# Optimization experiments

Hardware: AMD Instinct MI355X
Metric: run time of the kernel (lower is better)

Reference implementation:

```python
import jax, jax.numpy as jnp
import numpy as np

V, D, T_MAX, H, L = 32000, 1024, 1024, 16, 8
HD = D // H
DFF = 4 * D
EPS = 1e-5


def _pos_encoding(T, d_model, dtype=jnp.float32):
    pos = jnp.arange(T, dtype=jnp.float32)[:, None]                      # [T,1]
    div = jnp.exp(jnp.arange(0, d_model, 2, dtype=jnp.float32) * (-jnp.log(10000.0) / d_model))
    pe = jnp.zeros((T, d_model), dtype=jnp.float32)
    pe = pe.at[:, 0::2].set(jnp.sin(pos * div))
    pe = pe.at[:, 1::2].set(jnp.cos(pos * div))
    return pe.astype(dtype)


def _layernorm(x, g, b):
    mu = jnp.mean(x, axis=-1, keepdims=True)
    var = jnp.mean(jnp.square(x - mu), axis=-1, keepdims=True)
    return (x - mu) * jax.lax.rsqrt(var + EPS) * g + b


def setup_inputs() -> dict:
    key = jax.random.key(0)
    ks = jax.random.split(key, 9)
    s = 0.02
    return {
        "idx": jax.random.randint(ks[0], (2, 1024), 0, V),
        "embed": jax.random.normal(ks[1], (V, D), jnp.float32) * s,
        "Wqkv": jax.random.normal(ks[2], (L, D, 3 * D), jnp.float32) * s,
        "Wproj": jax.random.normal(ks[3], (L, D, D), jnp.float32) * s,
        "bproj": jnp.zeros((L, D), jnp.float32),
        "ln1_g": jnp.ones((L, D), jnp.float32),
        "ln1_b": jnp.zeros((L, D), jnp.float32),
        "ln2_g": jnp.ones((L, D), jnp.float32),
        "ln2_b": jnp.zeros((L, D), jnp.float32),
        "W1": jax.random.normal(ks[4], (L, D, DFF), jnp.float32) * s,
        "b1": jnp.zeros((L, DFF), jnp.float32),
        "W2": jax.random.normal(ks[5], (L, DFF, D), jnp.float32) * s,
        "b2": jnp.zeros((L, D), jnp.float32),
        "lnf_g": jnp.ones((D,), jnp.float32),
        "lnf_b": jnp.zeros((D,), jnp.float32),
        "Whead": jax.random.normal(ks[6], (D, V), jnp.float32) * s,
    }


def _attn(x, Wqkv, Wproj, bproj):
    B, T, C = x.shape
    qkv = (x @ Wqkv).reshape(B, T, 3, H, HD)
    q, k, v = [jnp.transpose(qkv[:, :, i], (0, 2, 1, 3)) for i in range(3)]  # [B,H,T,HD]
    scores = jnp.einsum('bhqd,bhkd->bhqk', q, k) * (HD ** -0.5)
    mask = jnp.tril(jnp.ones((T, T), dtype=bool))
    scores = jnp.where(mask, scores, -jnp.inf)
    w = jax.nn.softmax(scores, axis=-1)
    out = jnp.einsum('bhqk,bhkd->bhqd', w, v)
    out = jnp.transpose(out, (0, 2, 1, 3)).reshape(B, T, C)
    return out @ Wproj + bproj


def reference(idx, embed, Wqkv, Wproj, bproj, ln1_g, ln1_b, ln2_g, ln2_b,
              W1, b1, W2, b2, lnf_g, lnf_b, Whead):
    idx = idx[:, :T_MAX]
    T = idx.shape[1]
    x = embed[idx] + _pos_encoding(T, D)[None]          # [B,T,D]
    for l in range(L):
        x = x + _attn(_layernorm(x, ln1_g[l], ln1_b[l]), Wqkv[l], Wproj[l], bproj[l])
        h = _layernorm(x, ln2_g[l], ln2_b[l])
        x = x + jax.nn.relu(h @ W1[l] + b1[l]) @ W2[l] + b2[l]
    x = _layernorm(x, lnf_g, lnf_b)
    return x @ Whead                                     # [B,T,V]
```

## Files before the change

kernel.cpp:

```cpp
#include <hip/hip_runtime.h>
#include <cstddef>

#define DM    1024
#define TSEQ  1024
#define NB    2
#define NHEAD 16
#define HDIM  64
#define NLAYER 8
#define DFFN  4096
#define NVOC  32000
#define NROWS (NB*TSEQ)

typedef __attribute__((ext_vector_type(8))) short short8;
typedef __attribute__((ext_vector_type(4))) float f32x4;

static __device__ __forceinline__ unsigned short f2bf(float f) {
    union { float f; unsigned int u; } v; v.f = f;
    unsigned int r = v.u + 0x7FFF + ((v.u >> 16) & 1);
    return (unsigned short)(r >> 16);
}

static __device__ __forceinline__ void gload_lds16(const void* g, void* l) {
    __builtin_amdgcn_global_load_lds(
        (const __attribute__((address_space(1))) unsigned int*)g,
        (__attribute__((address_space(3))) unsigned int*)l, 16, 0, 0);
}

__global__ __launch_bounds__(256)
void embed_pos_k(const int* __restrict__ idx, const float* __restrict__ embed,
                 float* __restrict__ x)
{
    int row = blockIdx.x;
    int t   = row & (TSEQ - 1);
    int tid = threadIdx.x;
    int token = idx[row];
    const float* er = embed + (size_t)token * DM;
    float* xr = x + (size_t)row * DM;
    const float neg_ln1e4_over_d = -9.210340371976184f / (float)DM;
    for (int i = tid; i < DM; i += 256) {
        int half = i >> 1;
        float div = expf((float)(2 * half) * neg_ln1e4_over_d);
        float ang = (float)t * div;
        float pe = (i & 1) ? cosf(ang) : sinf(ang);
        xr[i] = er[i] + pe;
    }
}

__global__ __launch_bounds__(256)
void layernorm_k(const float* __restrict__ x, const float* __restrict__ g,
                 const float* __restrict__ b, unsigned short* __restrict__ y)
{
    int row = blockIdx.x;
    int tid = threadIdx.x;
    const float* xr = x + (size_t)row * DM;
    unsigned short* yr = y + (size_t)row * DM;
    float vals[4];
    float s = 0.f;
    #pragma unroll
    for (int i = 0; i < 4; ++i) { vals[i] = xr[tid + 256 * i]; s += vals[i]; }
    __shared__ float red[256];
    red[tid] = s; __syncthreads();
    for (int st = 128; st > 0; st >>= 1) {
        if (tid < st) red[tid] += red[tid + st];
        __syncthreads();
    }
    float mu = red[0] * (1.f / DM);
    __syncthreads();
    float v = 0.f;
    #pragma unroll
    for (int i = 0; i < 4; ++i) { float d = vals[i] - mu; v += d * d; }
    red[tid] = v; __syncthreads();
    for (int st = 128; st > 0; st >>= 1) {
        if (tid < st) red[tid] += red[tid + st];
        __syncthreads();
    }
    float rstd = rsqrtf(red[0] * (1.f / DM) + 1e-5f);
    #pragma unroll
    for (int i = 0; i < 4; ++i) {
        int c = tid + 256 * i;
        yr[c] = f2bf((vals[i] - mu) * rstd * g[c] + b[c]);
    }
}

__global__ __launch_bounds__(256)
void reduce_ln_k(const float* __restrict__ P, int nsplit, const float* __restrict__ bias,
                 float* __restrict__ X, const float* __restrict__ g,
                 const float* __restrict__ b, unsigned short* __restrict__ XN)
{
    const int row = blockIdx.x;
    const int tid = threadIdx.x;
    const size_t off4 = (size_t)row * 256 + tid;
    const size_t tot4 = (size_t)NROWS * 256;

    float4 v = *((const float4*)X + off4);
    float4 bb = *((const float4*)bias + tid);
    v.x += bb.x; v.y += bb.y; v.z += bb.z; v.w += bb.w;
    for (int s = 0; s < nsplit; ++s) {
        float4 p = *((const float4*)P + s * tot4 + off4);
        v.x += p.x; v.y += p.y; v.z += p.z; v.w += p.w;
    }
    *((float4*)X + off4) = v;

    __shared__ float red[256];
    red[tid] = v.x + v.y + v.z + v.w;
    __syncthreads();
    for (int st = 128; st > 0; st >>= 1) {
        if (tid < st) red[tid] += red[tid + st];
        __syncthreads();
    }
    float mu = red[0] * (1.f / DM);
    __syncthreads();
    float4 d = make_float4(v.x - mu, v.y - mu, v.z - mu, v.w - mu);
    red[tid] = d.x * d.x + d.y * d.y + d.z * d.z + d.w * d.w;
    __syncthreads();
    for (int st = 128; st > 0; st >>= 1) {
        if (tid < st) red[tid] += red[tid + st];
        __syncthreads();
    }
    float rstd = rsqrtf(red[0] * (1.f / DM) + 1e-5f);
    float4 gg = *((const float4*)g + tid);
    float4 bbn = *((const float4*)b + tid);
    unsigned short o[4];
    o[0] = f2bf(d.x * rstd * gg.x + bbn.x);
    o[1] = f2bf(d.y * rstd * gg.y + bbn.y);
    o[2] = f2bf(d.z * rstd * gg.z + bbn.z);
    o[3] = f2bf(d.w * rstd * gg.w + bbn.w);
    *(ushort4*)(XN + (size_t)row * DM + tid * 4) = *(ushort4*)o;
}

__global__ __launch_bounds__(256)
void convt_k(const float* __restrict__ src, unsigned short* __restrict__ dst,
             int K, int N)
{
    __shared__ __align__(16) unsigned short T[64][72];
    const int tid = threadIdx.x;
    const int n0 = blockIdx.x * 64, k0 = blockIdx.y * 64;
    const float* s = src + (size_t)blockIdx.z * K * N;
    unsigned short* d = dst + (size_t)blockIdx.z * K * N;
    #pragma unroll
    for (int q = 0; q < 4; ++q) {
        int f4 = tid + q * 256;
        int kk = f4 >> 4, nn = (f4 & 15) * 4;
        float4 v = *(const float4*)(s + (size_t)(k0 + kk) * N + n0 + nn);
        int swz = ((nn >> 2) & 7) << 3;
        T[nn + 0][kk ^ swz] = f2bf(v.x);
        T[nn + 1][kk ^ swz] = f2bf(v.y);
        T[nn + 2][kk ^ swz] = f2bf(v.z);
        T[nn + 3][kk ^ swz] = f2bf(v.w);
    }
    __syncthreads();
    #pragma unroll
    for (int q = 0; q < 2; ++q) {
        int s8 = tid + q * 256;
        int nn = s8 >> 3, kc = (s8 & 7) * 8;
        int swz = ((nn >> 2) & 7) << 3;
        *(short8*)(d + (size_t)(n0 + nn) * K + k0 + kc) =
            *(const short8*)&T[nn][kc ^ swz];
    }
}

template<int BM, int BN, bool OUT_BF16>
__global__ __launch_bounds__(256, 4)
void gemm_tn(const unsigned short* __restrict__ A, const unsigned short* __restrict__ BT,
             const float* __restrict__ bias, const float* __restrict__ residual,
             void* __restrict__ Cout, int M, int N, int K, int KS, int relu)
{
    constexpr int FRM = BM / 32;
    constexpr int FRN = BN / 32;
    constexpr int NIA = BM / 64;
    constexpr int NIB = BN / 64;
    constexpr int NLD = NIA + NIB;
    __shared__ __align__(16) unsigned short As[3][BM][32];
    __shared__ __align__(16) unsigned short Bs[3][BN][32];

    const int tid = threadIdx.x;
    const int lane = tid & 63;
    const int w = tid >> 6;
    const int wr = w >> 1, wc = w & 1;
    const int l16 = lane & 15, g = lane >> 4;

    const int nby = M / BM;
    const int nwg = (N / BN) * nby;
    const int cpx = nwg >> 3;
    const int bid = blockIdx.x;
    const int sbid = (bid & 7) * cpx + (bid >> 3);
    const int row0 = (sbid % nby) * BM;
    const int col0 = (sbid / nby) * BN;

    const int srowA = w * (BM / 4) + (lane >> 2);
    const int srowB = w * (BN / 4) + (lane >> 2);
    const int scol = (((lane & 3) ^ ((lane >> 3) & 3)) << 3);
    const int rslot = ((g ^ ((l16 >> 1) & 3)) << 3);
    const int ldst = (lane & 3) << 3;

    const unsigned short* ga = A  + (size_t)(row0 + srowA) * KS + (size_t)blockIdx.y * K + scol;
    const unsigned short* gb = BT + (size_t)(col0 + srowB) * KS + (size_t)blockIdx.y * K + scol;

    f32x4 acc[FRM][FRN] = {};
    const int NT = K >> 5;

    #pragma unroll
    for (int i = 0; i < NIA; ++i)
        gload_lds16(ga + (size_t)(i * 16) * KS, &As[0][srowA + i * 16][ldst]);
    #pragma unroll
    for (int i = 0; i < NIB; ++i)
        gload_lds16(gb + (size_t)(i * 16) * KS, &Bs[0][srowB + i * 16][ldst]);

    for (int t = 0; t < NT; ++t) {
        const int rb = t % 3;
        if (t + 1 < NT) {
            const int wb = (t + 1) % 3;
            const int ko = (t + 1) * 32;
            #pragma unroll
            for (int i = 0; i < NIA; ++i)
                gload_lds16(ga + ko + (size_t)(i * 16) * KS, &As[wb][srowA + i * 16][ldst]);
            #pragma unroll
            for (int i = 0; i < NIB; ++i)
                gload_lds16(gb + ko + (size_t)(i * 16) * KS, &Bs[wb][srowB + i * 16][ldst]);
            asm volatile("s_waitcnt vmcnt(%0)" :: "i"(NLD) : "memory");
        } else {
            asm volatile("s_waitcnt vmcnt(0)" ::: "memory");
        }
        __builtin_amdgcn_s_barrier();

        short8 af[FRM], bf[FRN];
        #pragma unroll
        for (int i = 0; i < FRM; ++i)
            af[i] = *(const short8*)&As[rb][wr * (BM / 2) + i * 16 + l16][rslot];
        #pragma unroll
        for (int j = 0; j < FRN; ++j)
            bf[j] = *(const short8*)&Bs[rb][wc * (BN / 2) + j * 16 + l16][rslot];
        __builtin_amdgcn_s_setprio(1);
        #pragma unroll
        for (int i = 0; i < FRM; ++i)
            #pragma unroll
            for (int j = 0; j < FRN; ++j)
                acc[i][j] = __builtin_amdgcn_mfma_f32_16x16x32_bf16(af[i], bf[j], acc[i][j], 0, 0, 0);
        __builtin_amdgcn_s_setprio(0);
    }

    float* Cf = (float*)Cout + (size_t)blockIdx.y * M * N;
    #pragma unroll
    for (int i = 0; i < FRM; ++i) {
        #pragma unroll
        for (int j = 0; j < FRN; ++j) {
            #pragma unroll
            for (int r = 0; r < 4; ++r) {
                int row = row0 + wr * (BM / 2) + i * 16 + g * 4 + r;
                int col = col0 + wc * (BN / 2) + j * 16 + l16;
                float v = acc[i][j][r];
                if (bias)     v += bias[col];
                if (residual) v += residual[(size_t)row * N + col];
                if (relu)     v = fmaxf(v, 0.f);
                if (OUT_BF16) ((unsigned short*)Cout)[(size_t)row * N + col] = f2bf(v);
                else          Cf[(size_t)row * N + col] = v;
            }
        }
    }
}

__global__ __launch_bounds__(256)
void attn_flash_k(const unsigned short* __restrict__ qkv, unsigned short* __restrict__ out)
{
    __shared__ unsigned short Ks[128][72];
    __shared__ unsigned short Vt[64][136];
    __shared__ unsigned short Ps[4][16][136];

    const int tid = threadIdx.x;
    const int lane = tid & 63;
    const int w = tid >> 6;
    const int l16 = lane & 15, g = lane >> 4;
    const int h = blockIdx.y;
    const int b = blockIdx.z;

    const size_t rstr = 3 * DM;
    const unsigned short* base = qkv + (size_t)b * TSEQ * rstr + h * HDIM;

    const int krow = tid >> 1, kcol = (tid & 1) * 32;
    const int vkv = tid & 127, vdh = (tid >> 7) * 32;

    short8 kreg[4], vreg[4];

    #pragma unroll
    for (int pass = 0; pass < 2; ++pass) {
        const int qb = pass ? (15 - (int)blockIdx.x) : (int)blockIdx.x;
        const int q0 = qb * 64;
        const int nt = (qb >> 1) + 1;

        const int qrow_w = q0 + w * 16 + l16;
        short8 aq0 = *(const short8*)(base + (size_t)qrow_w * rstr + g * 8);
        short8 aq1 = *(const short8*)(base + (size_t)qrow_w * rstr + 32 + g * 8);

        f32x4 acc_o[4] = {};
        float m_r[4] = {-INFINITY, -INFINITY, -INFINITY, -INFINITY};
        float l_r[4] = {};

        {
            const unsigned short* kb = base + (size_t)krow * rstr + DM + kcol;
            #pragma unroll
            for (int i = 0; i < 4; ++i) kreg[i] = *(const short8*)(kb + i * 8);
            const unsigned short* vb = base + (size_t)vkv * rstr + 2 * DM + vdh;
            #pragma unroll
            for (int i = 0; i < 4; ++i) vreg[i] = *(const short8*)(vb + i * 8);
        }

        for (int t = 0; t < nt; ++t) {
            #pragma unroll
            for (int i = 0; i < 4; ++i) *(short8*)&Ks[krow][kcol + i * 8] = kreg[i];
            #pragma unroll
            for (int jj = 0; jj < 4; ++jj)
                #pragma unroll
                for (int j = 0; j < 8; ++j)
                    Vt[vdh + jj * 8 + j][vkv] = (unsigned short)vreg[jj][j];
            __syncthreads();

            if (t + 1 < nt) {
                const int kv0n = (t + 1) * 128;
                const unsigned short* kb = base + (size_t)(kv0n + krow) * rstr + DM + kcol;
                #pragma unroll
                for (int i = 0; i < 4; ++i) kreg[i] = *(const short8*)(kb + i * 8);
                const unsigned short* vb = base + (size_t)(kv0n + vkv) * rstr + 2 * DM + vdh;
                #pragma unroll
                for (int i = 0; i < 4; ++i) vreg[i] = *(const short8*)(vb + i * 8);
            }

            const int kv0 = t * 128;
            f32x4 acc_s[8] = {};
            #pragma unroll
            for (int ks = 0; ks < 8; ++ks) {
                short8 bk0 = *(const short8*)&Ks[ks * 16 + l16][g * 8];
                short8 bk1 = *(const short8*)&Ks[ks * 16 + l16][32 + g * 8];
                acc_s[ks] = __builtin_amdgcn_mfma_f32_16x16x32_bf16(aq0, bk0, acc_s[ks], 0, 0, 0);
                acc_s[ks] = __builtin_amdgcn_mfma_f32_16x16x32_bf16(aq1, bk1, acc_s[ks], 0, 0, 0);
            }
            const bool need_mask = (kv0 + 127 > q0 + w * 16);
            float alpha[4];
            #pragma unroll
            for (int r = 0; r < 4; ++r) {
                const int q_abs = q0 + w * 16 + g * 4 + r;
                float s[8];
                #pragma unroll
                for (int ks = 0; ks < 8; ++ks) {
                    s[ks] = acc_s[ks][r] * 0.125f;
                    if (need_mask && (kv0 + ks * 16 + l16 > q_abs)) s[ks] = -INFINITY;
                }
                float pm = fmaxf(fmaxf(fmaxf(s[0], s[1]), fmaxf(s[2], s[3])),
                                 fmaxf(fmaxf(s[4], s[5]), fmaxf(s[6], s[7])));
                #pragma unroll
                for (int msk = 1; msk <= 8; msk <<= 1)
                    pm = fmaxf(pm, __shfl_xor(pm, msk));
                float mnew = fmaxf(m_r[r], pm);
                alpha[r] = __expf(m_r[r] - mnew);
                m_r[r] = mnew;
                float p[8], psum = 0.f;
                #pragma unroll
                for (int ks = 0; ks < 8; ++ks) {
                    p[ks] = (s[ks] == -INFINITY) ? 0.f : __expf(s[ks] - mnew);
                    psum += p[ks];
                }
                #pragma unroll
                for (int msk = 1; msk <= 8; msk <<= 1)
                    psum += __shfl_xor(psum, msk);
                l_r[r] = l_r[r] * alpha[r] + psum;
                #pragma unroll
                for (int ks = 0; ks < 8; ++ks)
                    Ps[w][g * 4 + r][ks * 16 + l16] = f2bf(p[ks]);
            }
            #pragma unroll
            for (int ds = 0; ds < 4; ++ds)
                #pragma unroll
                for (int r = 0; r < 4; ++r)
                    acc_o[ds][r] *= alpha[r];
            short8 ap[4];
            #pragma unroll
            for (int kk = 0; kk < 4; ++kk)
                ap[kk] = *(const short8*)&Ps[w][l16][kk * 32 + g * 8];
            #pragma unroll
            for (int ds = 0; ds < 4; ++ds) {
                #pragma unroll
                for (int kk = 0; kk < 4; ++kk) {
                    short8 bv = *(const short8*)&Vt[ds * 16 + l16][kk * 32 + g * 8];
                    acc_o[ds] = __builtin_amdgcn_mfma_f32_16x16x32_bf16(ap[kk], bv, acc_o[ds], 0, 0, 0);
                }
            }
            __syncthreads();
        }

        #pragma unroll
        for (int ds = 0; ds < 4; ++ds)
            #pragma unroll
            for (int r = 0; r < 4; ++r) {
                int row = q0 + w * 16 + g * 4 + r;
                out[((size_t)b * TSEQ + row) * DM + h * HDIM + ds * 16 + l16] =
                    f2bf(acc_o[ds][r] * (1.f / l_r[r]));
            }
    }
}

extern "C" void kernel_launch(void* const* d_in, const int* in_sizes, int n_in,
                              void* d_out, int out_size, void* d_ws, size_t ws_size,
                              hipStream_t stream)
{
    const int*   idx    = (const int*)  d_in[0];
    const float* embed  = (const float*)d_in[1];
    const float* Wqkv   = (const float*)d_in[2];
    const float* Wproj  = (const float*)d_in[3];
    const float* bproj  = (const float*)d_in[4];
    const float* ln1_g  = (const float*)d_in[5];
    const float* ln1_b  = (const float*)d_in[6];
    const float* ln2_g  = (const float*)d_in[7];
    const float* ln2_b  = (const float*)d_in[8];
    const float* W1     = (const float*)d_in[9];
    const float* b1     = (const float*)d_in[10];
    const float* W2     = (const float*)d_in[11];
    const float* b2     = (const float*)d_in[12];
    const float* lnf_g  = (const float*)d_in[13];
    const float* lnf_b  = (const float*)d_in[14];
    const float* Whead  = (const float*)d_in[15];
    float* out = (float*)d_out;

    float* X = (float*)d_ws;
    float* PK = X + (size_t)NROWS * DM;
    unsigned short* u = (unsigned short*)(PK + (size_t)4 * NROWS * DM);
    unsigned short* XN     = u;  u += (size_t)NROWS * DM;
    unsigned short* QKVb   = u;  u += (size_t)NROWS * 3 * DM;
    unsigned short* ATT    = u;  u += (size_t)NROWS * DM;
    unsigned short* FFH    = u;  u += (size_t)NROWS * DFFN;
    unsigned short* WqkvT  = u;  u += (size_t)NLAYER * 3 * DM * DM;
    unsigned short* WprojT = u;  u += (size_t)NLAYER * DM * DM;
    unsigned short* W1T    = u;  u += (size_t)NLAYER * DFFN * DM;
    unsigned short* W2T    = u;  u += (size_t)NLAYER * DM * DFFN;
    unsigned short* WheadT = u;  u += (size_t)NVOC * DM;

    convt_k<<<dim3(3 * DM / 64, DM / 64, NLAYER), 256, 0, stream>>>(Wqkv,  WqkvT,  DM,   3 * DM);
    convt_k<<<dim3(DM / 64,     DM / 64, NLAYER), 256, 0, stream>>>(Wproj, WprojT, DM,   DM);
    convt_k<<<dim3(DFFN / 64,   DM / 64, NLAYER), 256, 0, stream>>>(W1,    W1T,    DM,   DFFN);
    convt_k<<<dim3(DM / 64,   DFFN / 64, NLAYER), 256, 0, stream>>>(W2,    W2T,    DFFN, DM);
    convt_k<<<dim3(NVOC / 64,   DM / 64, 1),      256, 0, stream>>>(Whead, WheadT, DM,   NVOC);

    embed_pos_k<<<NROWS, 256, 0, stream>>>(idx, embed, X);
    layernorm_k<<<NROWS, 256, 0, stream>>>(X, ln1_g, ln1_b, XN);

    for (int l = 0; l < NLAYER; ++l) {
        const unsigned short* wqkvT_l  = WqkvT  + (size_t)l * 3 * DM * DM;
        const unsigned short* wprojT_l = WprojT + (size_t)l * DM * DM;
        const unsigned short* w1T_l    = W1T    + (size_t)l * DFFN * DM;
        const unsigned short* w2T_l    = W2T    + (size_t)l * DM * DFFN;
        const float* bproj_l = bproj + (size_t)l * DM;
        const float* b1_l = b1 + (size_t)l * DFFN;
        const float* b2_l = b2 + (size_t)l * DM;

        {
            int nwg = (NROWS / 128) * (3 * DM / 64);
            gemm_tn<128, 64, true><<<nwg, 256, 0, stream>>>(XN, wqkvT_l, nullptr, nullptr,
                                                            QKVb, NROWS, 3 * DM, DM, DM, 0);
        }
        {
            dim3 grid(TSEQ / 128, NHEAD, NB);
            attn_flash_k<<<grid, 256, 0, stream>>>(QKVb, ATT);
        }
        {
            dim3 grid((NROWS / 128) * (DM / 64), 2);
            gemm_tn<128, 64, false><<<grid, 256, 0, stream>>>(ATT, wprojT_l, nullptr, nullptr,
                                                              PK, NROWS, DM, 512, DM, 0);
            reduce_ln_k<<<NROWS, 256, 0, stream>>>(PK, 2, bproj_l, X,
                                                   ln2_g + (size_t)l * DM,
                                                   ln2_b + (size_t)l * DM, XN);
        }
        {
            int nwg = (NROWS / 128) * (DFFN / 64);
            gemm_tn<128, 64, true><<<nwg, 256, 0, stream>>>(XN, w1T_l, b1_l, nullptr,
                                                            FFH, NROWS, DFFN, DM, DM, 1);
        }
        {
            dim3 grid((NROWS / 128) * (DM / 64), 4);
            gemm_tn<128, 64, false><<<grid, 256, 0, stream>>>(FFH, w2T_l, nullptr, nullptr,
                                                              PK, NROWS, DM, 1024, DFFN, 0);
            const float* ng = (l + 1 < NLAYER) ? ln1_g + (size_t)(l + 1) * DM : lnf_g;
            const float* nb = (l + 1 < NLAYER) ? ln1_b + (size_t)(l + 1) * DM : lnf_b;
            reduce_ln_k<<<NROWS, 256, 0, stream>>>(PK, 4, b2_l, X, ng, nb, XN);
        }
    }

    {
        int nwg = (NROWS / 128) * (NVOC / 64);
        gemm_tn<128, 64, false><<<nwg, 256, 0, stream>>>(XN, WheadT, nullptr, nullptr,
                                                         out, NROWS, NVOC, DM, DM, 0);
    }
}
```

Baseline: 1.729 ms.

## Split attention into one q-block per workgroup and use 128x128 tiles for LM head

The attention kernel no longer runs two passes (q-block b and its mirror) per workgroup. It now launches 512 workgroups with a flat id that maps heavy q-blocks first, which gives more parallelism and a longest-first schedule. The online softmax now skips rescaling unless the max grows by more than 8, and it drops the explicit -inf check. The LM-head GEMM switches to a 128x128 tile variant without the occupancy hint, which raises data reuse per tile but may lower occupancy. The GEMM body is turned into a shared macro.

```diff
diff --git a/kernel.cpp b/kernel.cpp
--- a/kernel.cpp
+++ b/kernel.cpp
@@ -159,104 +159,107 @@
     }
 }
 
-template<int BM, int BN, bool OUT_BF16>
+#define GEMM_BODY(BM, BN)                                                        \
+    constexpr int FRM = (BM) / 32;                                               \
+    constexpr int FRN = (BN) / 32;                                               \
+    constexpr int NIA = (BM) / 64;                                               \
+    constexpr int NIB = (BN) / 64;                                               \
+    constexpr int NLD = NIA + NIB;                                               \
+    __shared__ __align__(16) unsigned short As[3][BM][32];                       \
+    __shared__ __align__(16) unsigned short Bs[3][BN][32];                       \
+    const int tid = threadIdx.x;                                                 \
+    const int lane = tid & 63;                                                   \
+    const int w = tid >> 6;                                                      \
+    const int wr = w >> 1, wc = w & 1;                                           \
+    const int l16 = lane & 15, g = lane >> 4;                                    \
+    const int nby = M / (BM);                                                    \
+    const int nwg = (N / (BN)) * nby;                                            \
+    const int cpx = nwg >> 3;                                                    \
+    const int bid = blockIdx.x;                                                  \
+    const int sbid = (bid & 7) * cpx + (bid >> 3);                               \
+    const int row0 = (sbid % nby) * (BM);                                        \
+    const int col0 = (sbid / nby) * (BN);                                        \
+    const int srowA = w * ((BM) / 4) + (lane >> 2);                              \
+    const int srowB = w * ((BN) / 4) + (lane >> 2);                              \
+    const int scol = (((lane & 3) ^ ((lane >> 3) & 3)) << 3);                    \
+    const int rslot = ((g ^ ((l16 >> 1) & 3)) << 3);                             \
+    const int ldst = (lane & 3) << 3;                                            \
+    const unsigned short* ga = A  + (size_t)(row0 + srowA) * KS + (size_t)blockIdx.y * K + scol; \
+    const unsigned short* gb = BT + (size_t)(col0 + srowB) * KS + (size_t)blockIdx.y * K + scol; \
+    f32x4 acc[FRM][FRN] = {};                                                    \
+    const int NT = K >> 5;                                                       \
+    _Pragma("unroll")                                                            \
+    for (int i = 0; i < NIA; ++i)                                                \
+        gload_lds16(ga + (size_t)(i * 16) * KS, &As[0][srowA + i * 16][ldst]);   \
+    _Pragma("unroll")                                                            \
+    for (int i = 0; i < NIB; ++i)                                                \
+        gload_lds16(gb + (size_t)(i * 16) * KS, &Bs[0][srowB + i * 16][ldst]);   \
+    for (int t = 0; t < NT; ++t) {                                               \
+        const int rb = t % 3;                                                    \
+        if (t + 1 < NT) {                                                        \
+            const int wb = (t + 1) % 3;                                          \
+            const int ko = (t + 1) * 32;                                         \
+            _Pragma("unroll")                                                    \
+            for (int i = 0; i < NIA; ++i)                                        \
+                gload_lds16(ga + ko + (size_t)(i * 16) * KS, &As[wb][srowA + i * 16][ldst]); \
+            _Pragma("unroll")                                                    \
+            for (int i = 0; i < NIB; ++i)                                        \
+                gload_lds16(gb + ko + (size_t)(i * 16) * KS, &Bs[wb][srowB + i * 16][ldst]); \
+            asm volatile("s_waitcnt vmcnt(%0)" :: "i"(NLD) : "memory");          \
+        } else {                                                                 \
+            asm volatile("s_waitcnt vmcnt(0)" ::: "memory");                     \
+        }                                                                        \
+        __builtin_amdgcn_s_barrier();                                            \
+        short8 af[FRM], bf[FRN];                                                 \
+        _Pragma("unroll")                                                        \
+        for (int i = 0; i < FRM; ++i)                                            \
+            af[i] = *(const short8*)&As[rb][wr * ((BM) / 2) + i * 16 + l16][rslot]; \
+        _Pragma("unroll")                                                        \
+        for (int j = 0; j < FRN; ++j)                                            \
+            bf[j] = *(const short8*)&Bs[rb][wc * ((BN) / 2) + j * 16 + l16][rslot]; \
+        __builtin_amdgcn_s_setprio(1);                                           \
+        _Pragma("unroll")                                                        \
+        for (int i = 0; i < FRM; ++i)                                            \
+            _Pragma("unroll")                                                    \
+            for (int j = 0; j < FRN; ++j)                                        \
+                acc[i][j] = __builtin_amdgcn_mfma_f32_16x16x32_bf16(af[i], bf[j], acc[i][j], 0, 0, 0); \
+        __builtin_amdgcn_s_setprio(0);                                           \
+    }                                                                            \
+    float* Cf = (float*)Cout + (size_t)blockIdx.y * M * N;                       \
+    _Pragma("unroll")                                                            \
+    for (int i = 0; i < FRM; ++i) {                                              \
+        _Pragma("unroll")                                                        \
+        for (int j = 0; j < FRN; ++j) {                                          \
+            _Pragma("unroll")                                                    \
+            for (int r = 0; r < 4; ++r) {                                        \
+                int row = row0 + wr * ((BM) / 2) + i * 16 + g * 4 + r;           \
+                int col = col0 + wc * ((BN) / 2) + j * 16 + l16;                 \
+                float v = acc[i][j][r];                                          \
+                if (bias)     v += bias[col];                                    \
+                if (residual) v += residual[(size_t)row * N + col];              \
+                if (relu)     v = fmaxf(v, 0.f);                                 \
+                if (OUT_BF16) ((unsigned short*)Cout)[(size_t)row * N + col] = f2bf(v); \
+                else          Cf[(size_t)row * N + col] = v;                     \
+            }                                                                    \
+        }                                                                        \
+    }
+
+template<bool OUT_BF16>
+__global__ __launch_bounds__(256)
+void gemm_big(const unsigned short* __restrict__ A, const unsigned short* __restrict__ BT,
+              const float* __restrict__ bias, const float* __restrict__ residual,
+              void* __restrict__ Cout, int M, int N, int K, int KS, int relu)
+{
+    GEMM_BODY(128, 128)
+}
+
+template<bool OUT_BF16>
 __global__ __launch_bounds__(256, 4)
-void gemm_tn(const unsigned short* __restrict__ A, const unsigned short* __restrict__ BT,
+void gemm_sm(const unsigned short* __restrict__ A, const unsigned short* __restrict__ BT,
              const float* __restrict__ bias, const float* __restrict__ residual,
              void* __restrict__ Cout, int M, int N, int K, int KS, int relu)
 {
-    constexpr int FRM = BM / 32;
-    constexpr int FRN = BN / 32;
-    constexpr int NIA = BM / 64;
-    constexpr int NIB = BN / 64;
-    constexpr int NLD = NIA + NIB;
-    __shared__ __align__(16) unsigned short As[3][BM][32];
-    __shared__ __align__(16) unsigned short Bs[3][BN][32];
-
-    const int tid = threadIdx.x;
-    const int lane = tid & 63;
-    const int w = tid >> 6;
-    const int wr = w >> 1, wc = w & 1;
-    const int l16 = lane & 15, g = lane >> 4;
-
-    const int nby = M / BM;
-    const int nwg = (N / BN) * nby;
-    const int cpx = nwg >> 3;
-    const int bid = blockIdx.x;
-    const int sbid = (bid & 7) * cpx + (bid >> 3);
-    const int row0 = (sbid % nby) * BM;
-    const int col0 = (sbid / nby) * BN;
-
-    const int srowA = w * (BM / 4) + (lane >> 2);
-    const int srowB = w * (BN / 4) + (lane >> 2);
-    const int scol = (((lane & 3) ^ ((lane >> 3) & 3)) << 3);
-    const int rslot = ((g ^ ((l16 >> 1) & 3)) << 3);
-    const int ldst = (lane & 3) << 3;
-
-    const unsigned short* ga = A  + (size_t)(row0 + srowA) * KS + (size_t)blockIdx.y * K + scol;
-    const unsigned short* gb = BT + (size_t)(col0 + srowB) * KS + (size_t)blockIdx.y * K + scol;
-
-    f32x4 acc[FRM][FRN] = {};
-    const int NT = K >> 5;
-
-    #pragma unroll
-    for (int i = 0; i < NIA; ++i)
-        gload_lds16(ga + (size_t)(i * 16) * KS, &As[0][srowA + i * 16][ldst]);
-    #pragma unroll
-    for (int i = 0; i < NIB; ++i)
-        gload_lds16(gb + (size_t)(i * 16) * KS, &Bs[0][srowB + i * 16][ldst]);
-
-    for (int t = 0; t < NT; ++t) {
-        const int rb = t % 3;
-        if (t + 1 < NT) {
-            const int wb = (t + 1) % 3;
-            const int ko = (t + 1) * 32;
-            #pragma unroll
-            for (int i = 0; i < NIA; ++i)
-                gload_lds16(ga + ko + (size_t)(i * 16) * KS, &As[wb][srowA + i * 16][ldst]);
-            #pragma unroll
-            for (int i = 0; i < NIB; ++i)
-                gload_lds16(gb + ko + (size_t)(i * 16) * KS, &Bs[wb][srowB + i * 16][ldst]);
-            asm volatile("s_waitcnt vmcnt(%0)" :: "i"(NLD) : "memory");
-        } else {
-            asm volatile("s_waitcnt vmcnt(0)" ::: "memory");
-        }
-        __builtin_amdgcn_s_barrier();
-
-        short8 af[FRM], bf[FRN];
-        #pragma unroll
-        for (int i = 0; i < FRM; ++i)
-            af[i] = *(const short8*)&As[rb][wr * (BM / 2) + i * 16 + l16][rslot];
-        #pragma unroll
-        for (int j = 0; j < FRN; ++j)
-            bf[j] = *(const short8*)&Bs[rb][wc * (BN / 2) + j * 16 + l16][rslot];
-        __builtin_amdgcn_s_setprio(1);
-        #pragma unroll
-        for (int i = 0; i < FRM; ++i)
-            #pragma unroll
-            for (int j = 0; j < FRN; ++j)
-                acc[i][j] = __builtin_amdgcn_mfma_f32_16x16x32_bf16(af[i], bf[j], acc[i][j], 0, 0, 0);
-        __builtin_amdgcn_s_setprio(0);
-    }
-
-    float* Cf = (float*)Cout + (size_t)blockIdx.y * M * N;
-    #pragma unroll
-    for (int i = 0; i < FRM; ++i) {
-        #pragma unroll
-        for (int j = 0; j < FRN; ++j) {
-            #pragma unroll
-            for (int r = 0; r < 4; ++r) {
-                int row = row0 + wr * (BM / 2) + i * 16 + g * 4 + r;
-                int col = col0 + wc * (BN / 2) + j * 16 + l16;
-                float v = acc[i][j][r];
-                if (bias)     v += bias[col];
-                if (residual) v += residual[(size_t)row * N + col];
-                if (relu)     v = fmaxf(v, 0.f);
-                if (OUT_BF16) ((unsigned short*)Cout)[(size_t)row * N + col] = f2bf(v);
-                else          Cf[(size_t)row * N + col] = v;
-            }
-        }
-    }
+    GEMM_BODY(128, 64)
 }
 
 __global__ __launch_bounds__(256)
@@ -270,8 +273,12 @@
     const int lane = tid & 63;
     const int w = tid >> 6;
     const int l16 = lane & 15, g = lane >> 4;
-    const int h = blockIdx.y;
-    const int b = blockIdx.z;
+
+    const int id = blockIdx.x;
+    const int qlow = id & 15;
+    const int qb = (id < 256) ? (15 - qlow) : qlow;
+    const int b = (id >> 4) & 1;
+    const int h = id >> 5;
 
     const size_t rstr = 3 * DM;
     const unsigned short* base = qkv + (size_t)b * TSEQ * rstr + h * HDIM;
@@ -279,122 +286,116 @@
     const int krow = tid >> 1, kcol = (tid & 1) * 32;
     const int vkv = tid & 127, vdh = (tid >> 7) * 32;
 
+    const int q0 = qb * 64;
+    const int nt = (qb >> 1) + 1;
+
+    const int qrow_w = q0 + w * 16 + l16;
+    short8 aq0 = *(const short8*)(base + (size_t)qrow_w * rstr + g * 8);
+    short8 aq1 = *(const short8*)(base + (size_t)qrow_w * rstr + 32 + g * 8);
+
+    f32x4 acc_o[4] = {};
+    float m_r[4] = {-INFINITY, -INFINITY, -INFINITY, -INFINITY};
+    float l_r[4] = {};
+
     short8 kreg[4], vreg[4];
-
-    #pragma unroll
-    for (int pass = 0; pass < 2; ++pass) {
-        const int qb = pass ? (15 - (int)blockIdx.x) : (int)blockIdx.x;
-        const int q0 = qb * 64;
-        const int nt = (qb >> 1) + 1;
-
-        const int qrow_w = q0 + w * 16 + l16;
-        short8 aq0 = *(const short8*)(base + (size_t)qrow_w * rstr + g * 8);
-        short8 aq1 = *(const short8*)(base + (size_t)qrow_w * rstr + 32 + g * 8);
-
-        f32x4 acc_o[4] = {};
-        float m_r[4] = {-INFINITY, -INFINITY, -INFINITY, -INFINITY};
-        float l_r[4] = {};
-
-        {
-            const unsigned short* kb = base + (size_t)krow * rstr + DM + kcol;
+    {
+        const unsigned short* kb = base + (size_t)krow * rstr + DM + kcol;
+        #pragma unroll
+        for (int i = 0; i < 4; ++i) kreg[i] = *(const short8*)(kb + i * 8);
+        const unsigned short* vb = base + (size_t)vkv * rstr + 2 * DM + vdh;
+        #pragma unroll
+        for (int i = 0; i < 4; ++i) vreg[i] = *(const short8*)(vb + i * 8);
+    }
+
+    for (int t = 0; t < nt; ++t) {
+        #pragma unroll
+        for (int i = 0; i < 4; ++i) *(short8*)&Ks[krow][kcol + i * 8] = kreg[i];
+        #pragma unroll
+        for (int jj = 0; jj < 4; ++jj)
+            #pragma unroll
+            for (int j = 0; j < 8; ++j)
+                Vt[vdh + jj * 8 + j][vkv] = (unsigned short)vreg[jj][j];
+        __syncthreads();
+
+        if (t + 1 < nt) {
+            const int kv0n = (t + 1) * 128;
+            const unsigned short* kb = base + (size_t)(kv0n + krow) * rstr + DM + kcol;
             #pragma unroll
             for (int i = 0; i < 4; ++i) kreg[i] = *(const short8*)(kb + i * 8);
-            const unsigned short* vb = base + (size_t)vkv * rstr + 2 * DM + vdh;
+            const unsigned short* vb = base + (size_t)(kv0n + vkv) * rstr + 2 * DM + vdh;
             #pragma unroll
             for (int i = 0; i < 4; ++i) vreg[i] = *(const short8*)(vb + i * 8);
         }
 
-        for (int t = 0; t < nt; ++t) {
-            #pragma unroll
-            for (int i = 0; i < 4; ++i) *(short8*)&Ks[krow][kcol + i * 8] = kreg[i];
-            #pragma unroll
-            for (int jj = 0; jj < 4; ++jj)
-                #pragma unroll
-                for (int j = 0; j < 8; ++j)
-                    Vt[vdh + jj * 8 + j][vkv] = (unsigned short)vreg[jj][j];
-            __syncthreads();
-
-            if (t + 1 < nt) {
-                const int kv0n = (t + 1) * 128;
-                const unsigned short* kb = base + (size_t)(kv0n + krow) * rstr + DM + kcol;
-                #pragma unroll
-                for (int i = 0; i < 4; ++i) kreg[i] = *(const short8*)(kb + i * 8);
-                const unsigned short* vb = base + (size_t)(kv0n + vkv) * rstr + 2 * DM + vdh;
-                #pragma unroll
-                for (int i = 0; i < 4; ++i) vreg[i] = *(const short8*)(vb + i * 8);
+        const int kv0 = t * 128;
+        f32x4 acc_s[8] = {};
+        #pragma unroll
+        for (int ks = 0; ks < 8; ++ks) {
+            short8 bk0 = *(const short8*)&Ks[ks * 16 + l16][g * 8];
+            short8 bk1 = *(const short8*)&Ks[ks * 16 + l16][32 + g * 8];
+            acc_s[ks] = __builtin_amdgcn_mfma_f32_16x16x32_bf16(aq0, bk0, acc_s[ks], 0, 0, 0);
+            acc_s[ks] = __builtin_amdgcn_mfma_f32_16x16x32_bf16(aq1, bk1, acc_s[ks], 0, 0, 0);
+        }
+        const bool need_mask = (kv0 + 127 > q0 + w * 16);
+        float alpha[4];
+        #pragma unroll
+        for (int r = 0; r < 4; ++r) {
+            const int q_abs = q0 + w * 16 + g * 4 + r;
+            float s[8];
+            #pragma unroll
+            for (int ks = 0; ks < 8; ++ks) {
+                s[ks] = acc_s[ks][r] * 0.125f;
+                if (need_mask && (kv0 + ks * 16 + l16 > q_abs)) s[ks] = -INFINITY;
             }
-
-            const int kv0 = t * 128;
-            f32x4 acc_s[8] = {};
+            float pm = fmaxf(fmaxf(fmaxf(s[0], s[1]), fmaxf(s[2], s[3])),
+                             fmaxf(fmaxf(s[4], s[5]), fmaxf(s[6], s[7])));
+            #pragma unroll
+            for (int msk = 1; msk <= 8; msk <<= 1)
+                pm = fmaxf(pm, __shfl_xor(pm, msk));
+            if (pm > m_r[r] + 8.f) { alpha[r] = __expf(m_r[r] - pm); m_r[r] = pm; }
+            else                   { alpha[r] = 1.f; }
+            float p[8], psum = 0.f;
             #pragma unroll
             for (int ks = 0; ks < 8; ++ks) {
-                short8 bk0 = *(const short8*)&Ks[ks * 16 + l16][g * 8];
-                short8 bk1 = *(const short8*)&Ks[ks * 16 + l16][32 + g * 8];
-                acc_s[ks] = __builtin_amdgcn_mfma_f32_16x16x32_bf16(aq0, bk0, acc_s[ks], 0, 0, 0);
-                acc_s[ks] = __builtin_amdgcn_mfma_f32_16x16x32_bf16(aq1, bk1, acc_s[ks], 0, 0, 0);
+                p[ks] = __expf(s[ks] - m_r[r]);
+                psum += p[ks];
             }
-            const bool need_mask = (kv0 + 127 > q0 + w * 16);
-            float alpha[4];
-            #pragma unroll
-            for (int r = 0; r < 4; ++r) {
-                const int q_abs = q0 + w * 16 + g * 4 + r;
-                float s[8];
-                #pragma unroll
-                for (int ks = 0; ks < 8; ++ks) {
-                    s[ks] = acc_s[ks][r] * 0.125f;
-                    if (need_mask && (kv0 + ks * 16 + l16 > q_abs)) s[ks] = -INFINITY;
-                }
-                float pm = fmaxf(fmaxf(fmaxf(s[0], s[1]), fmaxf(s[2], s[3])),
-                                 fmaxf(fmaxf(s[4], s[5]), fmaxf(s[6], s[7])));
-                #pragma unroll
-                for (int msk = 1; msk <= 8; msk <<= 1)
-                    pm = fmaxf(pm, __shfl_xor(pm, msk));
-                float mnew = fmaxf(m_r[r], pm);
-                alpha[r] = __expf(m_r[r] - mnew);
-                m_r[r] = mnew;
-                float p[8], psum = 0.f;
-                #pragma unroll
-                for (int ks = 0; ks < 8; ++ks) {
-                    p[ks] = (s[ks] == -INFINITY) ? 0.f : __expf(s[ks] - mnew);
-                    psum += p[ks];
-                }
-                #pragma unroll
-                for (int msk = 1; msk <= 8; msk <<= 1)
-                    psum += __shfl_xor(psum, msk);
-                l_r[r] = l_r[r] * alpha[r] + psum;
-                #pragma unroll
-                for (int ks = 0; ks < 8; ++ks)
-                    Ps[w][g * 4 + r][ks * 16 + l16] = f2bf(p[ks]);
+            #pragma unroll
+            for (int msk = 1; msk <= 8; msk <<= 1)
+                psum += __shfl_xor(psum, msk);
+            l_r[r] = l_r[r] * alpha[r] + psum;
+            #pragma unroll
+            for (int ks = 0; ks < 8; ++ks)
+                Ps[w][g * 4 + r][ks * 16 + l16] = f2bf(p[ks]);
+        }
+        #pragma unroll
+        for (int ds = 0; ds < 4; ++ds)
+            #pragma unroll
+            for (int r = 0; r < 4; ++r)
+                acc_o[ds][r] *= alpha[r];
+        short8 ap[4];
+        #pragma unroll
+        for (int kk = 0; kk < 4; ++kk)
+            ap[kk] = *(const short8*)&Ps[w][l16][kk * 32 + g * 8];
+        #pragma unroll
+        for (int ds = 0; ds < 4; ++ds) {
+            #pragma unroll
+            for (int kk = 0; kk < 4; ++kk) {
+                short8 bv = *(const short8*)&Vt[ds * 16 + l16][kk * 32 + g * 8];
+                acc_o[ds] = __builtin_amdgcn_mfma_f32_16x16x32_bf16(ap[kk], bv, acc_o[ds], 0, 0, 0);
             }
-            #pragma unroll
-            for (int ds = 0; ds < 4; ++ds)
-                #pragma unroll
-                for (int r = 0; r < 4; ++r)
-                    acc_o[ds][r] *= alpha[r];
-            short8 ap[4];
-            #pragma unroll
-            for (int kk = 0; kk < 4; ++kk)
-                ap[kk] = *(const short8*)&Ps[w][l16][kk * 32 + g * 8];
-            #pragma unroll
-            for (int ds = 0; ds < 4; ++ds) {
-                #pragma unroll
-                for (int kk = 0; kk < 4; ++kk) {
-                    short8 bv = *(const short8*)&Vt[ds * 16 + l16][kk * 32 + g * 8];
-                    acc_o[ds] = __builtin_amdgcn_mfma_f32_16x16x32_bf16(ap[kk], bv, acc_o[ds], 0, 0, 0);
-                }
-            }
-            __syncthreads();
-        }
-
-        #pragma unroll
-        for (int ds = 0; ds < 4; ++ds)
-            #pragma unroll
-            for (int r = 0; r < 4; ++r) {
-                int row = q0 + w * 16 + g * 4 + r;
-                out[((size_t)b * TSEQ + row) * DM + h * HDIM + ds * 16 + l16] =
-                    f2bf(acc_o[ds][r] * (1.f / l_r[r]));
-            }
-    }
+        }
+        __syncthreads();
+    }
+
+    #pragma unroll
+    for (int ds = 0; ds < 4; ++ds)
+        #pragma unroll
+        for (int r = 0; r < 4; ++r) {
+            int row = q0 + w * 16 + g * 4 + r;
+            out[((size_t)b * TSEQ + row) * DM + h * HDIM + ds * 16 + l16] =
+                f2bf(acc_o[ds][r] * (1.f / l_r[r]));
+        }
 }
 
 extern "C" void kernel_launch(void* const* d_in, const int* in_sizes, int n_in,
@@ -452,30 +453,29 @@
 
         {
             int nwg = (NROWS / 128) * (3 * DM / 64);
-            gemm_tn<128, 64, true><<<nwg, 256, 0, stream>>>(XN, wqkvT_l, nullptr, nullptr,
-                                                            QKVb, NROWS, 3 * DM, DM, DM, 0);
+            gemm_sm<true><<<nwg, 256, 0, stream>>>(XN, wqkvT_l, nullptr, nullptr,
+                                                   QKVb, NROWS, 3 * DM, DM, DM, 0);
         }
         {
-            dim3 grid(TSEQ / 128, NHEAD, NB);
-            attn_flash_k<<<grid, 256, 0, stream>>>(QKVb, ATT);
+            attn_flash_k<<<512, 256, 0, stream>>>(QKVb, ATT);
         }
         {
             dim3 grid((NROWS / 128) * (DM / 64), 2);
-            gemm_tn<128, 64, false><<<grid, 256, 0, stream>>>(ATT, wprojT_l, nullptr, nullptr,
-                                                              PK, NROWS, DM, 512, DM, 0);
+            gemm_sm<false><<<grid, 256, 0, stream>>>(ATT, wprojT_l, nullptr, nullptr,
+                                                     PK, NROWS, DM, 512, DM, 0);
             reduce_ln_k<<<NROWS, 256, 0, stream>>>(PK, 2, bproj_l, X,
                                                    ln2_g + (size_t)l * DM,
                                                    ln2_b + (size_t)l * DM, XN);
         }
         {
             int nwg = (NROWS / 128) * (DFFN / 64);
-            gemm_tn<128, 64, true><<<nwg, 256, 0, stream>>>(XN, w1T_l, b1_l, nullptr,
-                                                            FFH, NROWS, DFFN, DM, DM, 1);
+            gemm_sm<true><<<nwg, 256, 0, stream>>>(XN, w1T_l, b1_l, nullptr,
+                                                   FFH, NROWS, DFFN, DM, DM, 1);
         }
         {
             dim3 grid((NROWS / 128) * (DM / 64), 4);
-            gemm_tn<128, 64, false><<<grid, 256, 0, stream>>>(FFH, w2T_l, nullptr, nullptr,
-                                                              PK, NROWS, DM, 1024, DFFN, 0);
+            gemm_sm<false><<<grid, 256, 0, stream>>>(FFH, w2T_l, nullptr, nullptr,
+                                                     PK, NROWS, DM, 1024, DFFN, 0);
             const float* ng = (l + 1 < NLAYER) ? ln1_g + (size_t)(l + 1) * DM : lnf_g;
             const float* nb = (l + 1 < NLAYER) ? ln1_b + (size_t)(l + 1) * DM : lnf_b;
             reduce_ln_k<<<NROWS, 256, 0, stream>>>(PK, 4, b2_l, X, ng, nb, XN);
@@ -483,8 +483,8 @@
     }
 
     {
-        int nwg = (NROWS / 128) * (NVOC / 64);
-        gemm_tn<128, 64, false><<<nwg, 256, 0, stream>>>(XN, WheadT, nullptr, nullptr,
-                                                         out, NROWS, NVOC, DM, DM, 0);
-    }
-}
+        int nwg = (NROWS / 128) * (NVOC / 128);
+        gemm_big<false><<<nwg, 256, 0, stream>>>(XN, WheadT, nullptr, nullptr,
+                                                 out, NROWS, NVOC, DM, DM, 0);
+    }
+}
```

New measurement: 1.640 ms, median of 2. -5.1%, faster.
